# Optimization experiments

Hardware: AMD Instinct MI355X
Metric: run time of the kernel (lower is better)

## Reference

```python
import jax, jax.numpy as jnp
import numpy as np

N_NODES = 100000
N_EDGES = 200000
N_ATOM_FEATS = 56
HIDDEN = 256
N_GRAPHS = 2048
OUT_DIM = 1
EPS = 1e-5  # torch BatchNorm1d default


def setup_inputs() -> dict:
    key = jax.random.key(0)
    ks = jax.random.split(key, 10)
    x = jax.random.randint(ks[0], (N_NODES, N_ATOM_FEATS), 0, 2, dtype=jnp.int64 if jax.config.jax_enable_x64 else jnp.int32)
    edge_index = jax.random.randint(ks[1], (2, N_EDGES), 0, N_NODES)
    batch = jnp.sort(jax.random.randint(ks[2], (N_NODES,), 0, N_GRAPHS))
    emb_tables = jax.random.normal(ks[3], (N_ATOM_FEATS, 2, HIDDEN), dtype=jnp.float32) * 0.1
    Ws = jax.random.normal(ks[4], (3, HIDDEN, HIDDEN), dtype=jnp.float32) * (1.0 / np.sqrt(HIDDEN))
    bs = jnp.zeros((3, HIDDEN), dtype=jnp.float32)
    gammas = jnp.ones((2, HIDDEN), dtype=jnp.float32)
    betas = jnp.zeros((2, HIDDEN), dtype=jnp.float32)
    lin_w = jax.random.normal(ks[5], (HIDDEN, OUT_DIM), dtype=jnp.float32) * (1.0 / np.sqrt(HIDDEN))
    lin_b = jnp.zeros((OUT_DIM,), dtype=jnp.float32)
    return {"x": x, "edge_index": edge_index, "batch": batch, "emb_tables": emb_tables,
            "Ws": Ws, "bs": bs, "gammas": gammas, "betas": betas, "lin_w": lin_w, "lin_b": lin_b}


def reference(x, edge_index, batch, emb_tables, Ws, bs, gammas, betas, lin_w, lin_b):
    n = x.shape[0]
    # --- AtomEncoder: sum of 56 per-feature embedding lookups ---
    # emb_tables: [56, 2, H]; x: [N, 56] -> gathered [N, 56, H] -> sum over feature axis
    feat_idx = jnp.arange(x.shape[1])[None, :]  # [1,56]
    h = emb_tables[feat_idx, x].sum(axis=1)      # [N, H]

    # --- GCN normalization with self-loops (shared across layers) ---
    loops = jnp.arange(n)
    src = jnp.concatenate([edge_index[0], loops])
    dst = jnp.concatenate([edge_index[1], loops])
    deg = jax.ops.segment_sum(jnp.ones_like(src, dtype=h.dtype), dst, num_segments=n)
    dinv = jnp.where(deg > 0, jax.lax.rsqrt(deg), 0.0)
    norm = dinv[src] * dinv[dst]  # [E+N]

    def gcn_conv(h, W, b):
        hw = h @ W                                   # [N, H']
        msg = hw[src] * norm[:, None]                # gather + scale
        agg = jax.ops.segment_sum(msg, dst, num_segments=n)  # scatter-add
        return agg + b

    # --- layers 0..L-2: conv -> batchnorm (batch stats) -> relu; eval => no dropout ---
    for i in range(2):
        h = gcn_conv(h, Ws[i], bs[i])
        mu = h.mean(axis=0)
        var = h.var(axis=0)
        h = (h - mu) * jax.lax.rsqrt(var + EPS) * gammas[i] + betas[i]
        h = jax.nn.relu(h)
    # --- last conv (return_embeds=True: no softmax) ---
    h = gcn_conv(h, Ws[2], bs[2])

    # --- global mean pool over graphs ---
    sums = jax.ops.segment_sum(h, batch, num_segments=N_GRAPHS)          # [G, H]
    counts = jax.ops.segment_sum(jnp.ones((n,), h.dtype), batch, num_segments=N_GRAPHS)
    pooled = sums / jnp.maximum(counts, 1.0)[:, None]

    return pooled @ lin_w + lin_b  # [G, OUT_DIM]
```

## Files before the change

### kernel.cpp

```cpp
#include <hip/hip_runtime.h>
#include <hip/hip_bf16.h>

#define NN 100000
#define NE 200000
#define NF 56
#define HD 256
#define NG 2048

#define SCAN_CH 512
#define NCH ((NN + SCAN_CH - 1) / SCAN_CH)
#define EB ((NE + 255) / 256)

#define ZB 98
#define CVB ((NN + 255) / 256)
#define ENB ((NN + 127) / 128)
#define GM  32
#define GNB (NN / GM)

typedef __bf16 bf16x8 __attribute__((ext_vector_type(8)));
typedef __bf16 bf16x4 __attribute__((ext_vector_type(4)));
typedef float  floatx4 __attribute__((ext_vector_type(4)));

__global__ void prep_params(const float* __restrict__ emb, const float* __restrict__ Ws,
                            const float* __restrict__ bs, const float* __restrict__ lw,
                            __bf16* __restrict__ dW0t,
                            float* __restrict__ w2lw, float* __restrict__ b2lw,
                            __bf16* __restrict__ Wt, unsigned* __restrict__ deg,
                            const int* __restrict__ x, __bf16* __restrict__ xb) {
    __shared__ float row[HD];
    int c = threadIdx.x;
    int f = blockIdx.x;
    if (f >= NF + 2) {
        int g = f - (NF + 2);
        if (g < HD) {
            Wt[(size_t)g * HD + c] = (__bf16)Ws[(size_t)HD * HD + (size_t)c * HD + g];
        } else if (g < HD + ZB) {
            int idx = (g - HD) * HD + c;
            if (idx < NN / 4) ((int4*)deg)[idx] = make_int4(0, 0, 0, 0);
        } else {
            int r = (g - HD - ZB) * 256 + c;
            if (r < NN) {
                const int* xr = x + (size_t)r * NF;
                __bf16 o[64];
                #pragma unroll
                for (int j = 0; j < 14; ++j) {
                    int4 iv = *(const int4*)&xr[j * 4];
                    o[j * 4 + 0] = (__bf16)(float)iv.x;
                    o[j * 4 + 1] = (__bf16)(float)iv.y;
                    o[j * 4 + 2] = (__bf16)(float)iv.z;
                    o[j * 4 + 3] = (__bf16)(float)iv.w;
                }
                o[56] = (__bf16)1.0f;
                #pragma unroll
                for (int j = 57; j < 64; ++j) o[j] = (__bf16)0.0f;
                #pragma unroll
                for (int j = 0; j < 8; ++j)
                    *(bf16x8*)&xb[(size_t)r * 64 + j * 8] = *(const bf16x8*)&o[j * 8];
            }
        }
        return;
    }
    if (f == NF + 1) {
        const float* W2 = Ws + (size_t)2 * HD * HD;
        float acc = 0.f;
        for (int k = 0; k < HD; ++k) acc += W2[(size_t)c * HD + k] * lw[k];
        w2lw[c] = acc;
        row[c] = bs[2 * HD + c] * lw[c];
        __syncthreads();
        for (int off = 128; off > 0; off >>= 1) {
            if (c < off) row[c] += row[c + off];
            __syncthreads();
        }
        if (c == 0) *b2lw = row[0];
        return;
    }
    if (f < NF) {
        row[c] = emb[(f * 2 + 1) * HD + c] - emb[(f * 2 + 0) * HD + c];
    } else {
        float s = 0.f;
        for (int ff = 0; ff < NF; ++ff) s += emb[(ff * 2) * HD + c];
        row[c] = s;
    }
    __syncthreads();
    float acc = 0.f;
    for (int k = 0; k < HD; ++k) acc += row[k] * Ws[k * HD + c];
    if (f < NF) {
        dW0t[c * 64 + f] = (__bf16)acc;
    } else {
        dW0t[c * 64 + 56] = (__bf16)acc;
        #pragma unroll
        for (int k = 57; k < 64; ++k) dW0t[c * 64 + k] = (__bf16)0.f;
    }
}

__global__ void deg_kernel(const int* __restrict__ dst, unsigned* __restrict__ deg, int E) {
    int e = blockIdx.x * blockDim.x + threadIdx.x;
    if (e < E) atomicAdd(&deg[dst[e]], 1u);
}

__global__ void chunk_sum_dinv(const unsigned* __restrict__ deg, unsigned* __restrict__ csum,
                               float* __restrict__ dinv, float* __restrict__ selfn) {
    __shared__ unsigned s[SCAN_CH];
    int t = threadIdx.x;
    int base = blockIdx.x * SCAN_CH;
    unsigned v = (base + t < NN) ? deg[base + t] : 0u;
    s[t] = v;
    if (base + t < NN) {
        float d = (float)(v + 1u);
        dinv[base + t]  = rsqrtf(d);
        selfn[base + t] = 1.0f / d;
    }
    __syncthreads();
    for (int off = SCAN_CH / 2; off > 0; off >>= 1) {
        if (t < off) s[t] += s[t + off];
        __syncthreads();
    }
    if (t == 0) csum[blockIdx.x] = s[0];
}

__global__ void chunk_apply(const unsigned* __restrict__ deg, const unsigned* __restrict__ csum,
                            unsigned* __restrict__ row_start, unsigned* __restrict__ cursor) {
    __shared__ unsigned s[SCAN_CH];
    __shared__ unsigned cs[256];
    int t = threadIdx.x;
    if (t < 256) cs[t] = (t < NCH) ? csum[t] : 0u;
    __syncthreads();
    for (int off = 1; off < 256; off <<= 1) {
        unsigned add = (t < 256 && t >= off) ? cs[t - off] : 0u;
        __syncthreads();
        if (t < 256) cs[t] += add;
        __syncthreads();
    }
    unsigned chunk_base = (blockIdx.x == 0) ? 0u : cs[blockIdx.x - 1];

    int base = blockIdx.x * SCAN_CH;
    unsigned v = (base + t < NN) ? deg[base + t] : 0u;
    s[t] = v;
    __syncthreads();
    for (int off = 1; off < SCAN_CH; off <<= 1) {
        unsigned add = (t >= off) ? s[t - off] : 0u;
        __syncthreads();
        s[t] += add;
        __syncthreads();
    }
    if (base + t < NN) {
        unsigned rs = chunk_base + s[t] - v;
        row_start[base + t] = rs;
        cursor[base + t] = rs;
    }
    if (blockIdx.x == 0 && t == 0) row_start[NN] = NE;
}

__global__ void csr_fill_gb(const int* __restrict__ src, const int* __restrict__ dst,
                            const float* __restrict__ dinv, unsigned* __restrict__ cursor,
                            int* __restrict__ ecol, float* __restrict__ enorm,
                            const int* __restrict__ batch, unsigned* __restrict__ gstart) {
    int t = threadIdx.x;
    if (blockIdx.x < EB) {
        int e = blockIdx.x * 256 + t;
        if (e < NE) {
            int s = src[e], d = dst[e];
            unsigned pos = atomicAdd(&cursor[d], 1u);
            ecol[pos] = s;
            enorm[pos] = dinv[s] * dinv[d];
        }
    } else {
        int g = (blockIdx.x - EB) * 256 + t;
        if (g <= NG) {
            int lo = 0, hi = NN;
            while (lo < hi) {
                int mid = (lo + hi) >> 1;
                if (batch[mid] < g) lo = mid + 1; else hi = mid;
            }
            gstart[g] = (unsigned)lo;
        }
    }
}

#define ELSTR 68
__global__ void __launch_bounds__(512) enc_fused(const __bf16* __restrict__ xb,
                                                 const __bf16* __restrict__ dW0t,
                                                 const float* __restrict__ b0,
                                                 const float* __restrict__ selfn,
                                                 const unsigned* __restrict__ row_start,
                                                 const int* __restrict__ ecol,
                                                 const float* __restrict__ enorm,
                                                 __bf16* __restrict__ C,
                                                 float* __restrict__ part) {
    __shared__ __bf16 sA[128 * ELSTR];
    __shared__ __bf16 sB[256 * ELSTR];
    __shared__ float psum[8][64];
    __shared__ float psq[8][64];
    int t = threadIdx.x;
    int m0 = blockIdx.x * 128;
    int lane = t & 63, w = t >> 6;
    int quad = lane >> 4, l16 = lane & 15;
    int mw = (w & 1) * 64, nw = (w >> 1) * 64;

    {
        int bn = t >> 1;
        int kh = (t & 1) * 32;
        #pragma unroll
        for (int j = 0; j < 4; ++j)
            *(bf16x8*)&sB[bn * ELSTR + kh + j * 8] =
                *(const bf16x8*)&dW0t[(size_t)bn * 64 + kh + j * 8];
    }
    {
        int r = t >> 2;
        int p = (t & 3) * 16;
        int n = m0 + r;
        float acc[16];
        #pragma unroll
        for (int i = 0; i < 16; ++i) acc[i] = 0.f;
        if (n < NN) {
            float sn = selfn[n];
            bf16x8 a0 = *(const bf16x8*)&xb[(size_t)n * 64 + p];
            bf16x8 a1 = *(const bf16x8*)&xb[(size_t)n * 64 + p + 8];
            #pragma unroll
            for (int i = 0; i < 8; ++i) {
                acc[i]     = (float)a0[i] * sn;
                acc[8 + i] = (float)a1[i] * sn;
            }
            unsigned e0 = row_start[n], e1 = row_start[n + 1];
            unsigned e = e0;
            for (; e + 2 <= e1; e += 2) {
                int s0 = ecol[e], s1 = ecol[e + 1];
                float n0v = enorm[e], n1v = enorm[e + 1];
                bf16x8 u00 = *(const bf16x8*)&xb[(size_t)s0 * 64 + p];
                bf16x8 u01 = *(const bf16x8*)&xb[(size_t)s0 * 64 + p + 8];
                bf16x8 u10 = *(const bf16x8*)&xb[(size_t)s1 * 64 + p];
                bf16x8 u11 = *(const bf16x8*)&xb[(size_t)s1 * 64 + p + 8];
                #pragma unroll
                for (int i = 0; i < 8; ++i) {
                    acc[i]     += (float)u00[i] * n0v + (float)u10[i] * n1v;
                    acc[8 + i] += (float)u01[i] * n0v + (float)u11[i] * n1v;
                }
            }
            if (e < e1) {
                int s0 = ecol[e];
                float n0v = enorm[e];
                bf16x8 u00 = *(const bf16x8*)&xb[(size_t)s0 * 64 + p];
                bf16x8 u01 = *(const bf16x8*)&xb[(size_t)s0 * 64 + p + 8];
                #pragma unroll
                for (int i = 0; i < 8; ++i) {
                    acc[i]     += (float)u00[i] * n0v;
                    acc[8 + i] += (float)u01[i] * n0v;
                }
            }
        }
        bf16x8 o0, o1;
        #pragma unroll
        for (int i = 0; i < 8; ++i) { o0[i] = (__bf16)acc[i]; o1[i] = (__bf16)acc[8 + i]; }
        *(bf16x8*)&sA[r * ELSTR + p]     = o0;
        *(bf16x8*)&sA[r * ELSTR + p + 8] = o1;
    }
    __syncthreads();

    floatx4 acc[4][4] = {};
    #pragma unroll
    for (int s = 0; s < 2; ++s) {
        bf16x8 af[4], bfr[4];
        #pragma unroll
        for (int i = 0; i < 4; ++i)
            af[i] = *(const bf16x8*)&sA[(mw + i * 16 + l16) * ELSTR + s * 32 + quad * 8];
        #pragma unroll
        for (int i = 0; i < 4; ++i)
            bfr[i] = *(const bf16x8*)&sB[(nw + i * 16 + l16) * ELSTR + s * 32 + quad * 8];
        #pragma unroll
        for (int mi = 0; mi < 4; ++mi)
            #pragma unroll
            for (int ni = 0; ni < 4; ++ni)
                acc[mi][ni] = __builtin_amdgcn_mfma_f32_16x16x32_bf16(
                    af[mi], bfr[ni], acc[mi][ni], 0, 0, 0);
    }

    float bw[4];
    #pragma unroll
    for (int ni = 0; ni < 4; ++ni) bw[ni] = b0[nw + ni * 16 + l16];
    float ls[4] = {0.f, 0.f, 0.f, 0.f};
    float lq[4] = {0.f, 0.f, 0.f, 0.f};
    #pragma unroll
    for (int mi = 0; mi < 4; ++mi) {
        #pragma unroll
        for (int r = 0; r < 4; ++r) {
            int row = m0 + mw + mi * 16 + quad * 4 + r;
            if (row < NN) {
                #pragma unroll
                for (int ni = 0; ni < 4; ++ni) {
                    float v = acc[mi][ni][r] + bw[ni];
                    C[(size_t)row * HD + nw + ni * 16 + l16] = (__bf16)v;
                    ls[ni] += v;
                    lq[ni] += v * v;
                }
            }
        }
    }
    #pragma unroll
    for (int ni = 0; ni < 4; ++ni) {
        ls[ni] += __shfl_xor(ls[ni], 16, 64);
        ls[ni] += __shfl_xor(ls[ni], 32, 64);
        lq[ni] += __shfl_xor(lq[ni], 16, 64);
        lq[ni] += __shfl_xor(lq[ni], 32, 64);
    }
    if (lane < 16) {
        #pragma unroll
        for (int ni = 0; ni < 4; ++ni) {
            psum[w][ni * 16 + l16] = ls[ni];
            psq[w][ni * 16 + l16]  = lq[ni];
        }
    }
    __syncthreads();
    if (!(w & 1) && lane < 16) {
        #pragma unroll
        for (int ni = 0; ni < 4; ++ni) {
            int ci = ni * 16 + l16;
            part[(size_t)blockIdx.x * 512 + nw + ci]       = psum[w][ci] + psum[w + 1][ci];
            part[(size_t)blockIdx.x * 512 + 256 + nw + ci] = psq[w][ci]  + psq[w + 1][ci];
        }
    }
}

__global__ void __launch_bounds__(512) gcn_fused(const __bf16* __restrict__ h0,
                                                 const float* __restrict__ scale,
                                                 const float* __restrict__ shift,
                                                 const __bf16* __restrict__ Wt,
                                                 const float* __restrict__ b1,
                                                 const float* __restrict__ selfn,
                                                 const unsigned* __restrict__ row_start,
                                                 const int* __restrict__ ecol,
                                                 const float* __restrict__ enorm,
                                                 __bf16* __restrict__ C,
                                                 float* __restrict__ part) {
    __shared__ __bf16 sA[GM * 256];
    __shared__ __bf16 sB[256 * 36];
    int t = threadIdx.x;
    int m0 = blockIdx.x * GM;
    int lane = t & 63, w = t >> 6;
    int quad = lane >> 4, l16 = lane & 15;

    int bn = t >> 1, bk = (t & 1) * 16;
    bf16x8 pb[2];
    #pragma unroll
    for (int j = 0; j < 2; ++j)
        pb[j] = *(const bf16x8*)&Wt[(size_t)bn * HD + bk + j * 8];

    {
        int c4 = lane * 4;
        float4 sc = *(const float4*)&scale[c4];
        float4 sh = *(const float4*)&shift[c4];
        #pragma unroll
        for (int g = 0; g < 4; ++g) {
            int r = w * 4 + g;
            int n = m0 + r;
            float4 acc;
            float sn = selfn[n];
            bf16x4 hv = *(const bf16x4*)&h0[(size_t)n * HD + c4];
            acc.x = fmaxf((float)hv[0] * sc.x + sh.x, 0.f) * sn;
            acc.y = fmaxf((float)hv[1] * sc.y + sh.y, 0.f) * sn;
            acc.z = fmaxf((float)hv[2] * sc.z + sh.z, 0.f) * sn;
            acc.w = fmaxf((float)hv[3] * sc.w + sh.w, 0.f) * sn;
            unsigned e = row_start[n], e1 = row_start[n + 1];
            for (; e + 2 <= e1; e += 2) {
                int s0 = ecol[e], s1 = ecol[e + 1];
                float n0 = enorm[e], n1 = enorm[e + 1];
                bf16x4 u0 = *(const bf16x4*)&h0[(size_t)s0 * HD + c4];
                bf16x4 u1 = *(const bf16x4*)&h0[(size_t)s1 * HD + c4];
                acc.x += fmaxf((float)u0[0] * sc.x + sh.x, 0.f) * n0
                       + fmaxf((float)u1[0] * sc.x + sh.x, 0.f) * n1;
                acc.y += fmaxf((float)u0[1] * sc.y + sh.y, 0.f) * n0
                       + fmaxf((float)u1[1] * sc.y + sh.y, 0.f) * n1;
                acc.z += fmaxf((float)u0[2] * sc.z + sh.z, 0.f) * n0
                       + fmaxf((float)u1[2] * sc.z + sh.z, 0.f) * n1;
                acc.w += fmaxf((float)u0[3] * sc.w + sh.w, 0.f) * n0
                       + fmaxf((float)u1[3] * sc.w + sh.w, 0.f) * n1;
            }
            if (e < e1) {
                int s0 = ecol[e];
                float n0 = enorm[e];
                bf16x4 u0 = *(const bf16x4*)&h0[(size_t)s0 * HD + c4];
                acc.x += fmaxf((float)u0[0] * sc.x + sh.x, 0.f) * n0;
                acc.y += fmaxf((float)u0[1] * sc.y + sh.y, 0.f) * n0;
                acc.z += fmaxf((float)u0[2] * sc.z + sh.z, 0.f) * n0;
                acc.w += fmaxf((float)u0[3] * sc.w + sh.w, 0.f) * n0;
            }
            bf16x4 o;
            o[0] = (__bf16)acc.x; o[1] = (__bf16)acc.y;
            o[2] = (__bf16)acc.z; o[3] = (__bf16)acc.w;
            int swz = ((lane >> 1) ^ (r & 7));
            *(bf16x4*)&sA[r * 256 + swz * 8 + (lane & 1) * 4] = o;
        }
    }

    floatx4 cacc[2][2] = {};
    for (int k0 = 0; k0 < 256; k0 += 32) {
        *(bf16x8*)&sB[bn * 36 + bk]     = pb[0];
        *(bf16x8*)&sB[bn * 36 + bk + 8] = pb[1];
        __syncthreads();

        if (k0 + 32 < 256) {
            #pragma unroll
            for (int j = 0; j < 2; ++j)
                pb[j] = *(const bf16x8*)&Wt[(size_t)bn * HD + k0 + 32 + bk + j * 8];
        }

        bf16x8 af[2], bfr[2];
        int gbase = (k0 >> 3) + quad;
        #pragma unroll
        for (int mi = 0; mi < 2; ++mi) {
            int row = mi * 16 + l16;
            af[mi] = *(const bf16x8*)&sA[row * 256 + ((gbase ^ (l16 & 7)) << 3)];
        }
        #pragma unroll
        for (int ni = 0; ni < 2; ++ni)
            bfr[ni] = *(const bf16x8*)&sB[(w * 32 + ni * 16 + l16) * 36 + quad * 8];
        #pragma unroll
        for (int mi = 0; mi < 2; ++mi)
            #pragma unroll
            for (int ni = 0; ni < 2; ++ni)
                cacc[mi][ni] = __builtin_amdgcn_mfma_f32_16x16x32_bf16(
                    af[mi], bfr[ni], cacc[mi][ni], 0, 0, 0);
        __syncthreads();
    }

    float bw[2];
    #pragma unroll
    for (int ni = 0; ni < 2; ++ni) bw[ni] = b1[w * 32 + ni * 16 + l16];
    float ls[2] = {0.f, 0.f}, lq[2] = {0.f, 0.f};
    #pragma unroll
    for (int mi = 0; mi < 2; ++mi) {
        #pragma unroll
        for (int r_ = 0; r_ < 4; ++r_) {
            int row = m0 + mi * 16 + quad * 4 + r_;
            #pragma unroll
            for (int ni = 0; ni < 2; ++ni) {
                float v = cacc[mi][ni][r_] + bw[ni];
                C[(size_t)row * HD + w * 32 + ni * 16 + l16] = (__bf16)v;
                ls[ni] += v;
                lq[ni] += v * v;
            }
        }
    }
    #pragma unroll
    for (int ni = 0; ni < 2; ++ni) {
        ls[ni] += __shfl_xor(ls[ni], 16, 64);
        ls[ni] += __shfl_xor(ls[ni], 32, 64);
        lq[ni] += __shfl_xor(lq[ni], 16, 64);
        lq[ni] += __shfl_xor(lq[ni], 32, 64);
    }
    if (lane < 16) {
        #pragma unroll
        for (int ni = 0; ni < 2; ++ni) {
            int ci = w * 32 + ni * 16 + l16;
            part[(size_t)blockIdx.x * 512 + ci]       = ls[ni];
            part[(size_t)blockIdx.x * 512 + 256 + ci] = lq[ni];
        }
    }
}

__global__ void __launch_bounds__(256) bn_scale(const float* __restrict__ part, int nb,
                                                const float* __restrict__ gamma,
                                                const float* __restrict__ beta,
                                                float* __restrict__ scale,
                                                float* __restrict__ shift) {
    __shared__ float rs[256], rq[256];
    int t = threadIdx.x;
    int c = blockIdx.x;
    float s = 0.f, q = 0.f;
    for (int j = t; j < nb; j += 256) {
        s += part[(size_t)j * 512 + c];
        q += part[(size_t)j * 512 + 256 + c];
    }
    rs[t] = s; rq[t] = q;
    __syncthreads();
    for (int off = 128; off > 0; off >>= 1) {
        if (t < off) { rs[t] += rs[t + off]; rq[t] += rq[t + off]; }
        __syncthreads();
    }
    if (t == 0) {
        const float inv_n = 1.0f / (float)NN;
        float mu  = rs[0] * inv_n;
        float var = rq[0] * inv_n - mu * mu;
        float rstd = rsqrtf(var + 1e-5f);
        float sc = gamma[c] * rstd;
        scale[c] = sc;
        shift[c] = beta[c] - mu * sc;
    }
}

__global__ void __launch_bounds__(256) bn_dot(const __bf16* __restrict__ h,
                                              const float* __restrict__ scale,
                                              const float* __restrict__ shift,
                                              const float* __restrict__ w2lw,
                                              float* __restrict__ z) {
    int tid = blockIdx.x * 256 + threadIdx.x;
    int n = tid >> 6;
    if (n >= NN) return;
    int l = tid & 63;
    int c4 = l * 4;
    bf16x4 a = *(const bf16x4*)&h[(size_t)n * HD + c4];
    float4 sc = *(const float4*)&scale[c4];
    float4 sh = *(const float4*)&shift[c4];
    float4 wv = *(const float4*)&w2lw[c4];
    float d = fmaxf((float)a[0] * sc.x + sh.x, 0.f) * wv.x
            + fmaxf((float)a[1] * sc.y + sh.y, 0.f) * wv.y
            + fmaxf((float)a[2] * sc.z + sh.z, 0.f) * wv.z
            + fmaxf((float)a[3] * sc.w + sh.w, 0.f) * wv.w;
    #pragma unroll
    for (int off = 32; off > 0; off >>= 1) d += __shfl_down(d, off, 64);
    if (l == 0) z[n] = d;
}

__global__ void __launch_bounds__(256) pool_fused(const float* __restrict__ z,
                                                  const float* __restrict__ selfn,
                                                  const float* __restrict__ b2lw,
                                                  const unsigned* __restrict__ row_start,
                                                  const int* __restrict__ ecol,
                                                  const float* __restrict__ enorm,
                                                  const unsigned* __restrict__ gstart,
                                                  const float* __restrict__ lb,
                                                  float* __restrict__ out) {
    int tid = blockIdx.x * 256 + threadIdx.x;
    int g = tid >> 6;
    if (g >= NG) return;
    int l = tid & 63;
    unsigned s0 = gstart[g], s1 = gstart[g + 1];
    float bb = *b2lw;
    float s = 0.f;
    for (unsigned i = s0 + l; i < s1; i += 64) {
        float d = selfn[i] * z[i] + bb;
        unsigned e0 = row_start[i], e1 = row_start[i + 1];
        for (unsigned e = e0; e < e1; ++e)
            d += enorm[e] * z[ecol[e]];
        s += d;
    }
    #pragma unroll
    for (int off = 32; off > 0; off >>= 1) s += __shfl_down(s, off, 64);
    if (l == 0) out[g] = s / fmaxf((float)(s1 - s0), 1.0f) + lb[0];
}

extern "C" void kernel_launch(void* const* d_in, const int* in_sizes, int n_in,
                              void* d_out, int out_size, void* d_ws, size_t ws_size,
                              hipStream_t stream) {
    const int*   x     = (const int*)d_in[0];
    const int*   ei    = (const int*)d_in[1];
    const int*   batch = (const int*)d_in[2];
    const float* emb   = (const float*)d_in[3];
    const float* Ws    = (const float*)d_in[4];
    const float* bs    = (const float*)d_in[5];
    const float* gam   = (const float*)d_in[6];
    const float* bet   = (const float*)d_in[7];
    const float* lw    = (const float*)d_in[8];
    const float* lb    = (const float*)d_in[9];
    float* out = (float*)d_out;

    const int* src = ei;
    const int* dst = ei + NE;

    char* p = (char*)d_ws;
    size_t off = 0;
    auto carve = [&](size_t bytes) { void* r = p + off; off = (off + bytes + 255) & ~(size_t)255; return r; };
    __bf16*   buf0   = (__bf16*)carve((size_t)NN * HD * 2);
    __bf16*   buf1   = (__bf16*)carve((size_t)NN * HD * 2);
    __bf16*   xb     = (__bf16*)carve((size_t)NN * 64 * 2);
    __bf16*   dW0t   = (__bf16*)carve(HD * 64 * 2);
    __bf16*   Wt     = (__bf16*)carve((size_t)HD * HD * 2);
    float*    w2lw   = (float*)carve(HD * 4);
    float*    b2lw   = (float*)carve(256);
    unsigned* deg    = (unsigned*)carve(NN * 4);
    float*    dinv   = (float*)carve(NN * 4);
    float*    selfn  = (float*)carve(NN * 4);
    unsigned* csum   = (unsigned*)carve(256 * 4);
    unsigned* row_s  = (unsigned*)carve((NN + 1) * 4);
    unsigned* cursor = (unsigned*)carve(NN * 4);
    int*      ecol   = (int*)carve(NE * 4);
    float*    enorm  = (float*)carve(NE * 4);
    float*    part   = (float*)carve((size_t)GNB * 512 * 4);
    float*    scale  = (float*)carve(HD * 4);
    float*    shift  = (float*)carve(HD * 4);
    unsigned* gstart = (unsigned*)carve((NG + 1) * 4);
    float*    zbuf   = (float*)carve(NN * 4);
    (void)ws_size; (void)n_in; (void)in_sizes; (void)out_size;

    prep_params<<<NF + 2 + HD + ZB + CVB, HD, 0, stream>>>(
        emb, Ws, bs, lw, dW0t, w2lw, b2lw, Wt, deg, x, xb);

    deg_kernel<<<(NE + 255) / 256, 256, 0, stream>>>(dst, deg, NE);
    chunk_sum_dinv<<<NCH, SCAN_CH, 0, stream>>>(deg, csum, dinv, selfn);
    chunk_apply<<<NCH, SCAN_CH, 0, stream>>>(deg, csum, row_s, cursor);
    csr_fill_gb<<<EB + (NG + 256) / 256, 256, 0, stream>>>(
        src, dst, dinv, cursor, ecol, enorm, batch, gstart);

    enc_fused<<<ENB, 512, 0, stream>>>(
        xb, dW0t, bs, selfn, row_s, ecol, enorm, buf0, part);
    bn_scale<<<HD, 256, 0, stream>>>(part, ENB, gam, bet, scale, shift);

    gcn_fused<<<GNB, 512, 0, stream>>>(
        buf0, scale, shift, Wt, bs + HD, selfn, row_s, ecol, enorm, buf1, part);
    bn_scale<<<HD, 256, 0, stream>>>(part, GNB, gam + HD, bet + HD, scale, shift);

    bn_dot<<<(NN * 64 + 255) / 256, 256, 0, stream>>>(buf1, scale, shift, w2lw, zbuf);
    pool_fused<<<(NG * 64 + 255) / 256, 256, 0, stream>>>(
        zbuf, selfn, b2lw, row_s, ecol, enorm, gstart, lb, out);
}
```

Baseline: 256.3 us.

## Distribute block edges across waves with LDS atomics and keep weights in registers

The fused GCN kernel now spreads all of a block's edges evenly across its 8 waves. Each wave finds an edge's destination row by binary search over the block's row starts and accumulates into an fp32 LDS tile with atomicAdd, instead of each wave walking its own four rows' neighbor lists serially. This targets load imbalance from uneven degrees. The weight tile is now preloaded fully into registers, removing per-k-step LDS staging and barriers from the MFMA loop. The cost is LDS atomic contention, a larger fp32 tile plus a conversion pass, and higher register pressure from 16 bf16x8 weight fragments.

```diff
diff --git a/kernel.cpp b/kernel.cpp
--- a/kernel.cpp
+++ b/kernel.cpp
@@ -331,95 +331,98 @@
                                                  const float* __restrict__ enorm,
                                                  __bf16* __restrict__ C,
                                                  float* __restrict__ part) {
-    __shared__ __bf16 sA[GM * 256];
-    __shared__ __bf16 sB[256 * 36];
+    __shared__ float sAf[GM * 256];
+    __shared__ unsigned rs[GM + 1];
     int t = threadIdx.x;
     int m0 = blockIdx.x * GM;
     int lane = t & 63, w = t >> 6;
     int quad = lane >> 4, l16 = lane & 15;
-
-    int bn = t >> 1, bk = (t & 1) * 16;
-    bf16x8 pb[2];
-    #pragma unroll
-    for (int j = 0; j < 2; ++j)
-        pb[j] = *(const bf16x8*)&Wt[(size_t)bn * HD + bk + j * 8];
+    int c4 = lane * 4;
+
+    if (t <= GM) rs[t] = row_start[m0 + t];
+
+    bf16x8 breg[8][2];
+    #pragma unroll
+    for (int c = 0; c < 8; ++c)
+        #pragma unroll
+        for (int ni = 0; ni < 2; ++ni)
+            breg[c][ni] = *(const bf16x8*)&Wt[(size_t)(w * 32 + ni * 16 + l16) * HD + c * 32 + quad * 8];
+
+    float4 sc = *(const float4*)&scale[c4];
+    float4 sh = *(const float4*)&shift[c4];
+
+    #pragma unroll
+    for (int g = 0; g < 4; ++g) {
+        int r = w * 4 + g;
+        int n = m0 + r;
+        float sn = selfn[n];
+        bf16x4 hv = *(const bf16x4*)&h0[(size_t)n * HD + c4];
+        float* dp = &sAf[r * 256 + c4];
+        dp[0] = fmaxf((float)hv[0] * sc.x + sh.x, 0.f) * sn;
+        dp[1] = fmaxf((float)hv[1] * sc.y + sh.y, 0.f) * sn;
+        dp[2] = fmaxf((float)hv[2] * sc.z + sh.z, 0.f) * sn;
+        dp[3] = fmaxf((float)hv[3] * sc.w + sh.w, 0.f) * sn;
+    }
+    __syncthreads();
 
     {
-        int c4 = lane * 4;
-        float4 sc = *(const float4*)&scale[c4];
-        float4 sh = *(const float4*)&shift[c4];
-        #pragma unroll
-        for (int g = 0; g < 4; ++g) {
-            int r = w * 4 + g;
-            int n = m0 + r;
-            float4 acc;
-            float sn = selfn[n];
-            bf16x4 hv = *(const bf16x4*)&h0[(size_t)n * HD + c4];
-            acc.x = fmaxf((float)hv[0] * sc.x + sh.x, 0.f) * sn;
-            acc.y = fmaxf((float)hv[1] * sc.y + sh.y, 0.f) * sn;
-            acc.z = fmaxf((float)hv[2] * sc.z + sh.z, 0.f) * sn;
-            acc.w = fmaxf((float)hv[3] * sc.w + sh.w, 0.f) * sn;
-            unsigned e = row_start[n], e1 = row_start[n + 1];
-            for (; e + 2 <= e1; e += 2) {
-                int s0 = ecol[e], s1 = ecol[e + 1];
-                float n0 = enorm[e], n1 = enorm[e + 1];
-                bf16x4 u0 = *(const bf16x4*)&h0[(size_t)s0 * HD + c4];
-                bf16x4 u1 = *(const bf16x4*)&h0[(size_t)s1 * HD + c4];
-                acc.x += fmaxf((float)u0[0] * sc.x + sh.x, 0.f) * n0
-                       + fmaxf((float)u1[0] * sc.x + sh.x, 0.f) * n1;
-                acc.y += fmaxf((float)u0[1] * sc.y + sh.y, 0.f) * n0
-                       + fmaxf((float)u1[1] * sc.y + sh.y, 0.f) * n1;
-                acc.z += fmaxf((float)u0[2] * sc.z + sh.z, 0.f) * n0
-                       + fmaxf((float)u1[2] * sc.z + sh.z, 0.f) * n1;
-                acc.w += fmaxf((float)u0[3] * sc.w + sh.w, 0.f) * n0
-                       + fmaxf((float)u1[3] * sc.w + sh.w, 0.f) * n1;
-            }
-            if (e < e1) {
-                int s0 = ecol[e];
-                float n0 = enorm[e];
-                bf16x4 u0 = *(const bf16x4*)&h0[(size_t)s0 * HD + c4];
-                acc.x += fmaxf((float)u0[0] * sc.x + sh.x, 0.f) * n0;
-                acc.y += fmaxf((float)u0[1] * sc.y + sh.y, 0.f) * n0;
-                acc.z += fmaxf((float)u0[2] * sc.z + sh.z, 0.f) * n0;
-                acc.w += fmaxf((float)u0[3] * sc.w + sh.w, 0.f) * n0;
-            }
-            bf16x4 o;
-            o[0] = (__bf16)acc.x; o[1] = (__bf16)acc.y;
-            o[2] = (__bf16)acc.z; o[3] = (__bf16)acc.w;
-            int swz = ((lane >> 1) ^ (r & 7));
-            *(bf16x4*)&sA[r * 256 + swz * 8 + (lane & 1) * 4] = o;
-        }
-    }
-
+        unsigned r0 = rs[0], r2 = rs[GM];
+        auto edge_body = [&](unsigned e) {
+            int col = ecol[e];
+            float nm = enorm[e];
+            int lo = 0, hi = GM;
+            #pragma unroll
+            for (int it = 0; it < 5; ++it) {
+                int mid = (lo + hi) >> 1;
+                if (rs[mid] <= e) lo = mid; else hi = mid;
+            }
+            bf16x4 u = *(const bf16x4*)&h0[(size_t)col * HD + c4];
+            float* dp = &sAf[lo * 256 + c4];
+            atomicAdd(dp + 0, fmaxf((float)u[0] * sc.x + sh.x, 0.f) * nm);
+            atomicAdd(dp + 1, fmaxf((float)u[1] * sc.y + sh.y, 0.f) * nm);
+            atomicAdd(dp + 2, fmaxf((float)u[2] * sc.z + sh.z, 0.f) * nm);
+            atomicAdd(dp + 3, fmaxf((float)u[3] * sc.w + sh.w, 0.f) * nm);
+        };
+        unsigned e = r0 + w;
+        for (; e + 8 < r2; e += 16) { edge_body(e); edge_body(e + 8); }
+        if (e < r2) edge_body(e);
+    }
+    __syncthreads();
+
+    {
+        int r = t >> 4;
+        int c0 = (t & 15) * 16;
+        float tmp[16];
+        #pragma unroll
+        for (int i = 0; i < 16; ++i) tmp[i] = sAf[r * 256 + c0 + i];
+        __syncthreads();
+        __bf16* sA16w = (__bf16*)sAf;
+        bf16x8 o0, o1;
+        #pragma unroll
+        for (int i = 0; i < 8; ++i) { o0[i] = (__bf16)tmp[i]; o1[i] = (__bf16)tmp[8 + i]; }
+        int g0 = c0 >> 3;
+        *(bf16x8*)&sA16w[r * 256 + ((g0 ^ (r & 7)) << 3)]       = o0;
+        *(bf16x8*)&sA16w[r * 256 + (((g0 + 1) ^ (r & 7)) << 3)] = o1;
+    }
+    __syncthreads();
+
+    const __bf16* sA16 = (const __bf16*)sAf;
     floatx4 cacc[2][2] = {};
-    for (int k0 = 0; k0 < 256; k0 += 32) {
-        *(bf16x8*)&sB[bn * 36 + bk]     = pb[0];
-        *(bf16x8*)&sB[bn * 36 + bk + 8] = pb[1];
-        __syncthreads();
-
-        if (k0 + 32 < 256) {
-            #pragma unroll
-            for (int j = 0; j < 2; ++j)
-                pb[j] = *(const bf16x8*)&Wt[(size_t)bn * HD + k0 + 32 + bk + j * 8];
-        }
-
-        bf16x8 af[2], bfr[2];
-        int gbase = (k0 >> 3) + quad;
+    #pragma unroll
+    for (int c = 0; c < 8; ++c) {
+        bf16x8 af[2];
         #pragma unroll
         for (int mi = 0; mi < 2; ++mi) {
             int row = mi * 16 + l16;
-            af[mi] = *(const bf16x8*)&sA[row * 256 + ((gbase ^ (l16 & 7)) << 3)];
-        }
-        #pragma unroll
-        for (int ni = 0; ni < 2; ++ni)
-            bfr[ni] = *(const bf16x8*)&sB[(w * 32 + ni * 16 + l16) * 36 + quad * 8];
+            int g = (c * 4 + quad) ^ (l16 & 7);
+            af[mi] = *(const bf16x8*)&sA16[row * 256 + (g << 3)];
+        }
         #pragma unroll
         for (int mi = 0; mi < 2; ++mi)
             #pragma unroll
             for (int ni = 0; ni < 2; ++ni)
                 cacc[mi][ni] = __builtin_amdgcn_mfma_f32_16x16x32_bf16(
-                    af[mi], bfr[ni], cacc[mi][ni], 0, 0, 0);
-        __syncthreads();
+                    af[mi], breg[c][ni], cacc[mi][ni], 0, 0, 0);
     }
 
     float bw[2];
```

Measured after the change: 516.7 us. 2.02x slower.
